# Optimization experiments

Measured on AMD Instinct MI355X. Metric: run time of the kernel, lower is better.

## Reference

```python
import jax, jax.numpy as jnp
import numpy as np

B, T, H, W, D, NH = 8, 16, 14, 14, 768, 12
HID = int(D * 4.0)
HEAD_DIM = D // NH
EPS = 1e-5


def _ln(x, w, b):
    m = x.mean(-1, keepdims=True)
    v = ((x - m) ** 2).mean(-1, keepdims=True)
    return (x - m) * jax.lax.rsqrt(v + EPS) * w + b


def _attn(x, qkv_w, proj_w, proj_b):
    # x: [Bn, S, D]; qkv_w: [D, 3D] (no bias); proj: [D, D] + bias
    Bn, S, _ = x.shape
    qkv = (x @ qkv_w).reshape(Bn, S, 3, NH, HEAD_DIM).transpose(2, 0, 3, 1, 4)
    q, k, v = qkv[0], qkv[1], qkv[2]
    a = jnp.einsum('bhqd,bhkd->bhqk', q, k) * (HEAD_DIM ** -0.5)
    a = jax.nn.softmax(a, axis=-1)
    o = jnp.einsum('bhqk,bhkd->bhqd', a, v).transpose(0, 2, 1, 3).reshape(Bn, S, D)
    return o @ proj_w + proj_b


def setup_inputs() -> dict:
    key = jax.random.key(0)
    ks = jax.random.split(key, 20)
    N = H * W * T
    s = 0.02
    f32 = jnp.float32
    return {
        'x': jax.random.normal(ks[0], (B, 1 + N, D), f32),
        'tn1_w': jnp.ones((D,), f32), 'tn1_b': jnp.zeros((D,), f32),
        't_qkv_w': jax.random.normal(ks[1], (D, 3 * D), f32) * s,
        't_proj_w': jax.random.normal(ks[2], (D, D), f32) * s,
        't_proj_b': jnp.zeros((D,), f32),
        'tfc_w': jax.random.normal(ks[3], (D, D), f32) * s,
        'tfc_b': jnp.zeros((D,), f32),
        'n1_w': jnp.ones((D,), f32), 'n1_b': jnp.zeros((D,), f32),
        's_qkv_w': jax.random.normal(ks[4], (D, 3 * D), f32) * s,
        's_proj_w': jax.random.normal(ks[5], (D, D), f32) * s,
        's_proj_b': jnp.zeros((D,), f32),
        'n2_w': jnp.ones((D,), f32), 'n2_b': jnp.zeros((D,), f32),
        'fc1_w': jax.random.normal(ks[6], (D, HID), f32) * s,
        'fc1_b': jnp.zeros((HID,), f32),
        'fc2_w': jax.random.normal(ks[7], (HID, D), f32) * s,
        'fc2_b': jnp.zeros((D,), f32),
        'pt_mask': jnp.ones((B, 1 + N), dtype=bool),
        't_frames': T, 'height': H, 'width': W,
    }


def reference(x, tn1_w, tn1_b, t_qkv_w, t_proj_w, t_proj_b, tfc_w, tfc_b,
              n1_w, n1_b, s_qkv_w, s_proj_w, s_proj_b, n2_w, n2_b,
              fc1_w, fc1_b, fc2_w, fc2_b, pt_mask, t_frames, height, width):
    # divided space-time attention; USE_CLS_TOKEN=True, use_pt_visibility=False
    b = x.shape[0]
    t, h, w = t_frames, height, width
    n = h * w * t
    # --- temporal attention over t per (b, h, w) ---
    xt = x[:, 1:, :].reshape(b * h * w, t, D)  # 'b (h w t) m -> (b h w) t m'
    rt = _attn(_ln(xt, tn1_w, tn1_b), t_qkv_w, t_proj_w, t_proj_b)
    rt = rt.reshape(b, n, D) @ tfc_w + tfc_b  # temporal_fc
    xt2 = x[:, 1:, :] + rt
    init_cls = x[:, 0:1, :]  # [b, 1, D]
    # --- spatial attention over (1 + h*w) per (b, t) ---
    cls_tok = jnp.broadcast_to(init_cls, (b, t, D)).reshape(b * t, 1, D)
    xs = xt2.reshape(b, h * w, t, D).transpose(0, 2, 1, 3).reshape(b * t, h * w, D)
    xs = jnp.concatenate([cls_tok, xs], axis=1)  # [(b t), 1+hw, D]
    rs = _attn(_ln(xs, n1_w, n1_b), s_qkv_w, s_proj_w, s_proj_b)
    cls_out = rs[:, 0, :].reshape(b, t, D).mean(axis=1, keepdims=True)
    rs = rs[:, 1:, :].reshape(b, t, h * w, D).transpose(0, 2, 1, 3).reshape(b, n, D)
    x_new = jnp.concatenate([init_cls, xt2], axis=1) + jnp.concatenate([cls_out, rs], axis=1)
    # --- MLP block ---
    y = _ln(x_new, n2_w, n2_b)
    y = jax.nn.gelu(y @ fc1_w + fc1_b, approximate=False) @ fc2_w + fc2_b
    return x_new + y
```

## Files before the change

### kernel.cpp

```cpp
#include <hip/hip_runtime.h>
#include <cstdint>

using u16 = unsigned short;
using u32 = unsigned int;

typedef __bf16 bf16x8 __attribute__((ext_vector_type(8)));
typedef float  floatx4 __attribute__((ext_vector_type(4)));

#define DEV static __device__ __forceinline__

DEV u16 f2bf(float f) {
    u32 u = __float_as_uint(f);
    u += 0x7FFFu + ((u >> 16) & 1u);
    return (u16)(u >> 16);
}
DEV float bf2f(u16 v) { return __uint_as_float(((u32)v) << 16); }

DEV floatx4 mfma32(bf16x8 a, bf16x8 b, floatx4 c) {
    return __builtin_amdgcn_mfma_f32_16x16x32_bf16(a, b, c, 0, 0, 0);
}

DEV floatx4 fzero() { floatx4 z; z[0]=0.f; z[1]=0.f; z[2]=0.f; z[3]=0.f; return z; }

typedef __attribute__((address_space(3))) u32 as3_u32;
typedef __attribute__((address_space(1))) u32 as1_u32;

DEV void async_ld16(const u16* g, u16* l) {
    __builtin_amdgcn_global_load_lds(
        (const as1_u32*)g, (as3_u32*)l, 16, 0, 0);
}

__global__ __launch_bounds__(256) void transpose_w(
    const float* __restrict__ W, u16* __restrict__ Wt, int K, int N)
{
    __shared__ float t[32][33];
    const int tx = threadIdx.x, ty = threadIdx.y;
    const int gx = blockIdx.x * 32;
    const int gy = blockIdx.y * 32;
    #pragma unroll
    for (int i = 0; i < 4; ++i)
        t[ty + i*8][tx] = W[(size_t)(gy + ty + i*8) * N + gx + tx];
    __syncthreads();
    #pragma unroll
    for (int i = 0; i < 4; ++i)
        Wt[(size_t)(gx + ty + i*8) * K + gy + tx] = f2bf(t[tx][ty + i*8]);
}

template<int MODE>
__global__ __launch_bounds__(256) void ln_kernel(
    const float* __restrict__ xp, const u16* __restrict__ xt2,
    const float* __restrict__ w, const float* __restrict__ b,
    u16* __restrict__ out, int nrows)
{
    const int row = blockIdx.x * 4 + (threadIdx.x >> 6);
    if (row >= nrows) return;
    const int lane = threadIdx.x & 63;
    float vals[12];
    if constexpr (MODE == 0) {
        const float* src = xp + (size_t)(row + row/3136 + 1) * 768;
        #pragma unroll
        for (int j = 0; j < 3; ++j) {
            float4 v = reinterpret_cast<const float4*>(src)[j*64 + lane];
            vals[j*4+0]=v.x; vals[j*4+1]=v.y; vals[j*4+2]=v.z; vals[j*4+3]=v.w;
        }
    } else {
        const int bt = row / 197;
        const int p  = row - bt * 197;
        const int b0 = bt >> 4, tt = bt & 15;
        if (p == 0) {
            const float* src = xp + (size_t)b0 * 3137 * 768;
            #pragma unroll
            for (int j = 0; j < 3; ++j) {
                float4 v = reinterpret_cast<const float4*>(src)[j*64 + lane];
                vals[j*4+0]=v.x; vals[j*4+1]=v.y; vals[j*4+2]=v.z; vals[j*4+3]=v.w;
            }
        } else {
            const u16* src = xt2 + (size_t)(b0*3136 + (p-1)*16 + tt) * 768;
            #pragma unroll
            for (int j = 0; j < 3; ++j) {
                uint2 q = reinterpret_cast<const uint2*>(src)[j*64 + lane];
                vals[j*4+0] = bf2f((u16)(q.x & 0xFFFF));
                vals[j*4+1] = bf2f((u16)(q.x >> 16));
                vals[j*4+2] = bf2f((u16)(q.y & 0xFFFF));
                vals[j*4+3] = bf2f((u16)(q.y >> 16));
            }
        }
    }
    float s = 0.f, ss = 0.f;
    #pragma unroll
    for (int e = 0; e < 12; ++e) { s += vals[e]; ss += vals[e]*vals[e]; }
    #pragma unroll
    for (int o = 32; o > 0; o >>= 1) { s += __shfl_xor(s, o); ss += __shfl_xor(ss, o); }
    const float mean = s * (1.f/768.f);
    const float var  = ss * (1.f/768.f) - mean*mean;
    const float rstd = rsqrtf(var + 1e-5f);
    #pragma unroll
    for (int j = 0; j < 3; ++j) {
        const int c4 = (j*64 + lane) * 4;
        union { u16 u[4]; uint2 q; } o;
        #pragma unroll
        for (int e = 0; e < 4; ++e)
            o.u[e] = f2bf((vals[j*4+e] - mean)*rstd*w[c4+e] + b[c4+e]);
        *reinterpret_cast<uint2*>(&out[(size_t)row*768 + c4]) = o.q;
    }
}

__global__ __launch_bounds__(256) void combine_ln2(
    const float* __restrict__ xp, const u16* __restrict__ xt2,
    const u16* __restrict__ rsb, const float* __restrict__ w, const float* __restrict__ b,
    float* __restrict__ xnew, u16* __restrict__ ln2, int nrows)
{
    const int row = blockIdx.x * 4 + (threadIdx.x >> 6);
    if (row >= nrows) return;
    const int lane = threadIdx.x & 63;
    const int b0 = row / 3137;
    const int j  = row - b0 * 3137;
    float vals[12];
    if (j == 0) {
        #pragma unroll
        for (int e = 0; e < 12; ++e) {
            const int c = e*64 + lane;
            float acc = 0.f;
            for (int t = 0; t < 16; ++t)
                acc += bf2f(rsb[(size_t)(b0*16 + t) * 197 * 768 + c]);
            vals[e] = xp[(size_t)row*768 + c] + acc * (1.f/16.f);
        }
    } else {
        const int n_idx = j - 1;
        const int hw = n_idx >> 4, tt = n_idx & 15;
        const u16* a  = xt2 + (size_t)(b0*3136 + n_idx) * 768;
        const u16* r2 = rsb + (size_t)((b0*16 + tt)*197 + 1 + hw) * 768;
        #pragma unroll
        for (int e = 0; e < 12; ++e) {
            const int c = e*64 + lane;
            vals[e] = bf2f(a[c]) + bf2f(r2[c]);
        }
    }
    float s = 0.f, ss = 0.f;
    #pragma unroll
    for (int e = 0; e < 12; ++e) { s += vals[e]; ss += vals[e]*vals[e]; }
    #pragma unroll
    for (int o = 32; o > 0; o >>= 1) { s += __shfl_xor(s, o); ss += __shfl_xor(ss, o); }
    const float mean = s * (1.f/768.f);
    const float var  = ss * (1.f/768.f) - mean*mean;
    const float rstd = rsqrtf(var + 1e-5f);
    #pragma unroll
    for (int e = 0; e < 12; ++e) {
        const int c = e*64 + lane;
        xnew[(size_t)row*768 + c] = vals[e];
        ln2[(size_t)row*768 + c]  = f2bf((vals[e] - mean)*rstd*w[c] + b[c]);
    }
}

template<int RESID, bool BIAS, bool GELU_ACT, bool OUTF, bool OUTB, bool MASKM>
__global__ __launch_bounds__(256) void gemm_bt(
    const u16* __restrict__ A, const u16* __restrict__ Bt,
    const float* __restrict__ bias, const float* __restrict__ resid,
    float* __restrict__ Cf, u16* __restrict__ Cb,
    int N, int K, int lda, int ldb, int Mvalid)
{
    __shared__ __attribute__((aligned(16))) u16 smem[2*128*32];
    u16* As = smem;
    u16* Bs = smem + 128*32;
    const int tid  = threadIdx.x;
    const int wave = tid >> 6;
    const int lane = tid & 63;
    const int m15  = lane & 15;
    const int quad = lane >> 4;
    const int wm = wave >> 1, wn = wave & 1;
    const long m0 = (long)blockIdx.y * 128;
    const long n0 = (long)blockIdx.x * 128;

    const int s0 = wave*128 + lane;
    const int s1 = s0 + 64;
    const int kc0 = (s0 & 3) ^ ((s0 >> 3) & 3);
    const int kc1 = (s1 & 3) ^ ((s1 >> 3) & 3);
    const u16* Ag0 = A  + (size_t)(m0 + (s0 >> 2)) * lda + kc0 * 8;
    const u16* Ag1 = A  + (size_t)(m0 + (s1 >> 2)) * lda + kc1 * 8;
    const u16* Bg0 = Bt + (size_t)(n0 + (s0 >> 2)) * ldb + kc0 * 8;
    const u16* Bg1 = Bt + (size_t)(n0 + (s1 >> 2)) * ldb + kc1 * 8;
    u16* Al0 = &As[(wave*2 + 0) * 512];
    u16* Al1 = &As[(wave*2 + 1) * 512];
    u16* Bl0 = &Bs[(wave*2 + 0) * 512];
    u16* Bl1 = &Bs[(wave*2 + 1) * 512];

    const int swz = (quad ^ ((m15 >> 1) & 3)) * 8;

    floatx4 acc[4][4];
    #pragma unroll
    for (int i = 0; i < 4; ++i)
        #pragma unroll
        for (int j = 0; j < 4; ++j) acc[i][j] = fzero();

    for (int k0 = 0; k0 < K; k0 += 32) {
        __syncthreads();
        async_ld16(Ag0 + k0, Al0);
        async_ld16(Ag1 + k0, Al1);
        async_ld16(Bg0 + k0, Bl0);
        async_ld16(Bg1 + k0, Bl1);
        __syncthreads();
        bf16x8 af[4], bf[4];
        #pragma unroll
        for (int i = 0; i < 4; ++i)
            af[i] = *reinterpret_cast<const bf16x8*>(&As[(wm*64 + i*16 + m15)*32 + swz]);
        #pragma unroll
        for (int j = 0; j < 4; ++j)
            bf[j] = *reinterpret_cast<const bf16x8*>(&Bs[(wn*64 + j*16 + m15)*32 + swz]);
        #pragma unroll
        for (int i = 0; i < 4; ++i)
            #pragma unroll
            for (int j = 0; j < 4; ++j)
                acc[i][j] = mfma32(af[i], bf[j], acc[i][j]);
    }

    float bv[4];
    #pragma unroll
    for (int j = 0; j < 4; ++j)
        bv[j] = BIAS ? bias[n0 + wn*64 + j*16 + m15] : 0.f;

    if constexpr (OUTB) {
        u16* cbuf = smem + wave * 2048;
        #pragma unroll
        for (int p = 0; p < 2; ++p) {
            __syncthreads();
            #pragma unroll
            for (int ii = 0; ii < 2; ++ii) {
                const int i = p*2 + ii;
                #pragma unroll
                for (int j = 0; j < 4; ++j) {
                    #pragma unroll
                    for (int r = 0; r < 4; ++r) {
                        const long row = m0 + wm*64 + i*16 + quad*4 + r;
                        float v = acc[i][j][r] + bv[j];
                        if constexpr (RESID == 1)
                            v += resid[(size_t)row * N + (n0 + wn*64 + j*16 + m15)];
                        if constexpr (RESID == 2)
                            v += resid[(size_t)(row + row/3136 + 1) * 768 + (n0 + wn*64 + j*16 + m15)];
                        if constexpr (GELU_ACT)
                            v = 0.5f * v * (1.f + erff(v * 0.70710678118f));
                        cbuf[(ii*16 + quad*4 + r)*64 + j*16 + m15] = f2bf(v);
                    }
                }
            }
            __syncthreads();
            #pragma unroll
            for (int it = 0; it < 4; ++it) {
                const int lr = (lane >> 3) + it*8;
                const int cc = lane & 7;
                const uint4 val = *reinterpret_cast<const uint4*>(&cbuf[lr*64 + cc*8]);
                const long grow = m0 + wm*64 + p*32 + lr;
                *reinterpret_cast<uint4*>(&Cb[(size_t)grow * N + n0 + wn*64 + cc*8]) = val;
            }
        }
    } else {
        #pragma unroll
        for (int j = 0; j < 4; ++j) {
            const long col = n0 + wn*64 + j*16 + m15;
            #pragma unroll
            for (int i = 0; i < 4; ++i) {
                const long rowb = m0 + wm*64 + i*16 + quad*4;
                #pragma unroll
                for (int r = 0; r < 4; ++r) {
                    const long row = rowb + r;
                    if constexpr (MASKM) { if (row >= Mvalid) continue; }
                    float v = acc[i][j][r] + bv[j];
                    if constexpr (RESID == 1) v += resid[(size_t)row * N + col];
                    if constexpr (RESID == 2) v += resid[(size_t)(row + row/3136 + 1) * 768 + col];
                    if constexpr (GELU_ACT)   v = 0.5f * v * (1.f + erff(v * 0.70710678118f));
                    if constexpr (OUTF) Cf[(size_t)row * N + col] = v;
                }
            }
        }
    }
}

template<int S, int NQ, int NIT>
__global__ __launch_bounds__(256) void attn_kernel(
    const u16* __restrict__ qkv, u16* __restrict__ out, int ntask)
{
    __shared__ __attribute__((aligned(16))) u16 P_lds[4][16*32];
    const int wave = threadIdx.x >> 6;
    const int lane = threadIdx.x & 63;
    const int task = blockIdx.x * 4 + wave;
    if (task >= ntask) return;
    const int seq  = task / (12 * NQ);
    const int rem  = task - seq * (12 * NQ);
    const int head = rem / NQ;
    const int qt   = rem - head * NQ;
    const int m15  = lane & 15;
    const int quad = lane >> 4;
    const size_t base = (size_t)seq * S;

    const u16* qp = qkv + (base + qt*16 + m15) * 2304 + head*64 + quad*8;
    const bf16x8 Qf0 = *reinterpret_cast<const bf16x8*>(qp);
    const bf16x8 Qf1 = *reinterpret_cast<const bf16x8*>(qp + 32);

    floatx4 Oacc[4];
    #pragma unroll
    for (int c = 0; c < 4; ++c) Oacc[c] = fzero();
    float mrun = -__builtin_inff();
    float lrun = 0.f;
    u16* P = &P_lds[wave][0];

    for (int it = 0; it < NIT; ++it) {
        const int j0 = it * 32;
        floatx4 st[2];
        #pragma unroll
        for (int h2 = 0; h2 < 2; ++h2) {
            const u16* kp = qkv + (base + j0 + h2*16 + m15) * 2304 + 768 + head*64 + quad*8;
            const bf16x8 K0 = *reinterpret_cast<const bf16x8*>(kp);
            const bf16x8 K1 = *reinterpret_cast<const bf16x8*>(kp + 32);
            floatx4 z = fzero();
            z = mfma32(K0, Qf0, z);
            st[h2] = mfma32(K1, Qf1, z);
        }
        float sc[8];
        #pragma unroll
        for (int h2 = 0; h2 < 2; ++h2)
            #pragma unroll
            for (int r = 0; r < 4; ++r) {
                const int jj = j0 + h2*16 + quad*4 + r;
                sc[h2*4+r] = (jj < S) ? st[h2][r] * 0.125f : -__builtin_inff();
            }
        float tmax = sc[0];
        #pragma unroll
        for (int k = 1; k < 8; ++k) tmax = fmaxf(tmax, sc[k]);
        tmax = fmaxf(tmax, __shfl_xor(tmax, 16));
        tmax = fmaxf(tmax, __shfl_xor(tmax, 32));
        const float mnew = fmaxf(mrun, tmax);
        float p[8], tsum = 0.f;
        #pragma unroll
        for (int k = 0; k < 8; ++k) { p[k] = __expf(sc[k] - mnew); tsum += p[k]; }
        tsum += __shfl_xor(tsum, 16);
        tsum += __shfl_xor(tsum, 32);
        const float alpha = __expf(mrun - mnew);
        lrun = lrun * alpha + tsum;
        mrun = mnew;
        #pragma unroll
        for (int r = 0; r < 4; ++r) {
            const float ar = __shfl(alpha, quad*4 + r);
            #pragma unroll
            for (int c = 0; c < 4; ++c) Oacc[c][r] *= ar;
        }
        #pragma unroll
        for (int h2 = 0; h2 < 2; ++h2)
            #pragma unroll
            for (int r = 0; r < 4; ++r)
                P[m15*32 + h2*16 + quad*4 + r] = f2bf(p[h2*4+r]);
        const bf16x8 Pf = *reinterpret_cast<const bf16x8*>(&P[m15*32 + quad*8]);
        #pragma unroll
        for (int c = 0; c < 4; ++c) {
            union { u16 u[8]; bf16x8 v; } vf;
            #pragma unroll
            for (int jj2 = 0; jj2 < 8; ++jj2)
                vf.u[jj2] = qkv[(base + j0 + quad*8 + jj2) * 2304 + 1536 + head*64 + c*16 + m15];
            Oacc[c] = mfma32(Pf, vf.v, Oacc[c]);
        }
    }
    const float linv_self = 1.f / lrun;
    #pragma unroll
    for (int r = 0; r < 4; ++r) {
        const int prow = qt*16 + quad*4 + r;
        const float linv = __shfl(linv_self, quad*4 + r);
        if (prow < S) {
            u16* op = out + (base + prow) * 768 + head*64 + m15;
            #pragma unroll
            for (int c = 0; c < 4; ++c) op[c*16] = f2bf(Oacc[c][r] * linv);
        }
    }
}

extern "C" void kernel_launch(void* const* d_in, const int* in_sizes, int n_in,
                              void* d_out, int out_size, void* d_ws, size_t ws_size,
                              hipStream_t stream)
{
    (void)in_sizes; (void)n_in; (void)out_size; (void)ws_size;
    const float* x        = (const float*)d_in[0];
    const float* tn1_w    = (const float*)d_in[1];
    const float* tn1_b    = (const float*)d_in[2];
    const float* t_qkv_w  = (const float*)d_in[3];
    const float* t_proj_w = (const float*)d_in[4];
    const float* t_proj_b = (const float*)d_in[5];
    const float* tfc_w    = (const float*)d_in[6];
    const float* tfc_b    = (const float*)d_in[7];
    const float* n1_w     = (const float*)d_in[8];
    const float* n1_b     = (const float*)d_in[9];
    const float* s_qkv_w  = (const float*)d_in[10];
    const float* s_proj_w = (const float*)d_in[11];
    const float* s_proj_b = (const float*)d_in[12];
    const float* n2_w     = (const float*)d_in[13];
    const float* n2_b     = (const float*)d_in[14];
    const float* fc1_w    = (const float*)d_in[15];
    const float* fc1_b    = (const float*)d_in[16];
    const float* fc2_w    = (const float*)d_in[17];
    const float* fc2_b    = (const float*)d_in[18];
    float* out = (float*)d_out;

    char* ws = (char*)d_ws;
    size_t off = 0;
    auto alloc = [&](size_t bytes) -> void* {
        void* p = ws + off;
        off += (bytes + 255) & ~(size_t)255;
        return p;
    };
    u16* wt_tqkv  = (u16*)alloc((size_t)768*2304*2);
    u16* wt_tproj = (u16*)alloc((size_t)768*768*2);
    u16* wt_tfc   = (u16*)alloc((size_t)768*768*2);
    u16* wt_sqkv  = (u16*)alloc((size_t)768*2304*2);
    u16* wt_sproj = (u16*)alloc((size_t)768*768*2);
    u16* wt_fc1   = (u16*)alloc((size_t)768*3072*2);
    u16* wt_fc2   = (u16*)alloc((size_t)3072*768*2);
    u16* slotA = (u16*)alloc((size_t)25280*2304*2);
    u16* slotB = (u16*)alloc((size_t)25216*768*2);
    u16* slotD = (u16*)alloc((size_t)25216*768*2);
    u16* slotE = (u16*)alloc((size_t)25216*768*2);

    dim3 tb(32, 8);
    transpose_w<<<dim3(72, 24), tb, 0, stream>>>(t_qkv_w,  wt_tqkv,  768, 2304);
    transpose_w<<<dim3(24, 24), tb, 0, stream>>>(t_proj_w, wt_tproj, 768, 768);
    transpose_w<<<dim3(24, 24), tb, 0, stream>>>(tfc_w,    wt_tfc,   768, 768);
    transpose_w<<<dim3(72, 24), tb, 0, stream>>>(s_qkv_w,  wt_sqkv,  768, 2304);
    transpose_w<<<dim3(24, 24), tb, 0, stream>>>(s_proj_w, wt_sproj, 768, 768);
    transpose_w<<<dim3(96, 24), tb, 0, stream>>>(fc1_w,    wt_fc1,   768, 3072);
    transpose_w<<<dim3(24, 96), tb, 0, stream>>>(fc2_w,    wt_fc2,   3072, 768);

    u16* lnT  = slotD;
    u16* qkvT = slotA;
    ln_kernel<0><<<25088/4, 256, 0, stream>>>(x, nullptr, tn1_w, tn1_b, lnT, 25088);
    gemm_bt<0,false,false,false,true,false><<<dim3(18,196), 256, 0, stream>>>(
        lnT, wt_tqkv, nullptr, nullptr, nullptr, qkvT, 2304, 768, 768, 768, 0);

    u16* attnT = slotD;
    attn_kernel<16,1,1><<<18816/4, 256, 0, stream>>>(qkvT, attnT, 18816);

    u16* hp = slotE;
    gemm_bt<0,true,false,false,true,false><<<dim3(6,196), 256, 0, stream>>>(
        attnT, wt_tproj, t_proj_b, nullptr, nullptr, hp, 768, 768, 768, 768, 0);

    u16* xt2 = slotB;
    gemm_bt<2,true,false,false,true,false><<<dim3(6,196), 256, 0, stream>>>(
        hp, wt_tfc, tfc_b, x, nullptr, xt2, 768, 768, 768, 768, 0);

    u16* lnS = slotD;
    ln_kernel<1><<<25216/4, 256, 0, stream>>>(x, xt2, n1_w, n1_b, lnS, 25216);

    u16* qkvS = slotA;
    gemm_bt<0,false,false,false,true,false><<<dim3(18,197), 256, 0, stream>>>(
        lnS, wt_sqkv, nullptr, nullptr, nullptr, qkvS, 2304, 768, 768, 768, 0);

    u16* attnS = slotD;
    attn_kernel<197,13,7><<<19968/4, 256, 0, stream>>>(qkvS, attnS, 19968);

    u16* rsb = slotE;
    gemm_bt<0,true,false,false,true,false><<<dim3(6,197), 256, 0, stream>>>(
        attnS, wt_sproj, s_proj_b, nullptr, nullptr, rsb, 768, 768, 768, 768, 0);

    float* xnew = out;
    u16* ln2 = slotD;
    combine_ln2<<<25096/4, 256, 0, stream>>>(x, xt2, rsb, n2_w, n2_b, xnew, ln2, 25096);

    u16* h1 = slotA;
    for (int half = 0; half < 2; ++half) {
        const u16* w1h = wt_fc1 + (size_t)half * 1536 * 768;
        const float* b1h = fc1_b + half * 1536;
        gemm_bt<0,true,true,false,true,false><<<dim3(12,197), 256, 0, stream>>>(
            ln2, w1h, b1h, nullptr, nullptr, h1, 1536, 768, 768, 768, 0);
        const u16* w2h = wt_fc2 + (size_t)half * 1536;
        if (half == 0)
            gemm_bt<1,true,false,true,false,true><<<dim3(6,197), 256, 0, stream>>>(
                h1, w2h, fc2_b, out, out, nullptr, 768, 1536, 1536, 3072, 25096);
        else
            gemm_bt<1,false,false,true,false,true><<<dim3(6,197), 256, 0, stream>>>(
                h1, w2h, nullptr, out, out, nullptr, 768, 1536, 1536, 3072, 25096);
    }
}
```

Baseline: 1.417 ms.

## Replace 128x128 GEMM with 256x256 double-buffered pipelined 8-wave kernel

Replaces the 4-wave 128x128 GEMM, which synchronised around every 32-wide K step, with a 512-thread 256x256 tile kernel. It uses 64-wide K stages double-buffered in 128KB of dynamic LDS, interleaves async global loads with MFMA quarters, and adds explicit waitcnt, sched barriers and setprio. The goal is to hide load latency and raise operand reuse per byte loaded. In exchange it adds M-masking for partial tiles, padding of one slot, and heavy register and LDS pressure that may limit occupancy.

Result: faster. 1.297 ms (-8.4%).

```diff
diff --git a/kernel.cpp b/kernel.cpp
--- a/kernel.cpp
+++ b/kernel.cpp
@@ -152,118 +152,172 @@
     }
 }
 
+
+#define BARX() do { __builtin_amdgcn_sched_barrier(0); asm volatile("" ::: "memory"); \
+    __builtin_amdgcn_s_barrier(); asm volatile("" ::: "memory"); \
+    __builtin_amdgcn_sched_barrier(0); } while(0)
+#define WAITL() do { asm volatile("s_waitcnt lgkmcnt(0)" ::: "memory"); \
+    __builtin_amdgcn_sched_barrier(0); } while(0)
+#define WAITV4() do { asm volatile("s_waitcnt vmcnt(4)" ::: "memory"); \
+    __builtin_amdgcn_sched_barrier(0); } while(0)
+#define WAITV0() do { asm volatile("s_waitcnt vmcnt(0)" ::: "memory"); \
+    __builtin_amdgcn_sched_barrier(0); } while(0)
+
+#define RD_A(d, mh) do { \
+    _Pragma("unroll") for (int ff = 0; ff < 4; ++ff) { \
+      _Pragma("unroll") for (int ks = 0; ks < 2; ++ks) { \
+        const int rr = ((mh)*4 + ff)*16 + m15; \
+        a[ff*2+ks] = *reinterpret_cast<const bf16x8*>( \
+            &sm[(d)*32768 + wm*8192 + rr*64 + ((ks*4 + quad) ^ (m15 & 7))*8]); \
+    } } } while(0)
+
+#define RD_B(d, np) do { \
+    _Pragma("unroll") for (int nn = 0; nn < 2; ++nn) { \
+      _Pragma("unroll") for (int ks = 0; ks < 2; ++ks) { \
+        const int rr = (wn & 1)*64 + ((np)*2 + nn)*16 + m15; \
+        b[((np)*2 + nn)*2 + ks] = *reinterpret_cast<const bf16x8*>( \
+            &sm[(d)*32768 + 16384 + (wn >> 1)*8192 + rr*64 + ((ks*4 + quad) ^ (m15 & 7))*8]); \
+    } } } while(0)
+
+#define MQ(F0, NF0) do { \
+    _Pragma("unroll") for (int ff = 0; ff < 4; ++ff) { \
+      _Pragma("unroll") for (int nn = 0; nn < 2; ++nn) { \
+        floatx4 c_ = acc[(F0)+ff][(NF0)+nn]; \
+        c_ = mfma32(a[ff*2+0], b[((NF0)+nn)*2+0], c_); \
+        c_ = mfma32(a[ff*2+1], b[((NF0)+nn)*2+1], c_); \
+        acc[(F0)+ff][(NF0)+nn] = c_; \
+    } } } while(0)
+
+#define PRIO1() __builtin_amdgcn_s_setprio(1)
+#define PRIO0() __builtin_amdgcn_s_setprio(0)
+
+#define ITER(tt, FULL) do { \
+    const int d_ = (tt) & 1; \
+     RD_A(d_, 0); RD_B(d_, 0); STAGE((tt)+1, 2); \
+    BARX(); WAITL(); PRIO1(); MQ(0,0); PRIO0(); BARX(); \
+     RD_B(d_, 1); STAGE((tt)+1, 3); \
+    BARX(); WAITL(); PRIO1(); MQ(0,2); PRIO0(); BARX(); \
+     RD_A(d_, 1); if (FULL) STAGE((tt)+2, 0); \
+    BARX(); WAITL(); PRIO1(); MQ(4,2); PRIO0(); BARX(); \
+     if (FULL) STAGE((tt)+2, 1); \
+    BARX(); PRIO1(); MQ(4,0); PRIO0(); \
+    if (FULL) WAITV4(); else WAITV0(); \
+    BARX(); \
+     RD_A(d_^1, 0); RD_B(d_^1, 0); if (FULL) STAGE((tt)+2, 2); \
+    BARX(); WAITL(); PRIO1(); MQ(0,0); PRIO0(); BARX(); \
+     RD_B(d_^1, 1); if (FULL) STAGE((tt)+2, 3); \
+    BARX(); WAITL(); PRIO1(); MQ(0,2); PRIO0(); BARX(); \
+     RD_A(d_^1, 1); if (FULL) STAGE((tt)+3, 0); \
+    BARX(); WAITL(); PRIO1(); MQ(4,2); PRIO0(); BARX(); \
+     if (FULL) STAGE((tt)+3, 1); \
+    BARX(); PRIO1(); MQ(4,0); PRIO0(); \
+    if (FULL) WAITV4(); \
+    BARX(); \
+} while(0)
+
 template<int RESID, bool BIAS, bool GELU_ACT, bool OUTF, bool OUTB, bool MASKM>
-__global__ __launch_bounds__(256) void gemm_bt(
+__global__ __launch_bounds__(512, 2) void gemm256(
     const u16* __restrict__ A, const u16* __restrict__ Bt,
     const float* __restrict__ bias, const float* __restrict__ resid,
     float* __restrict__ Cf, u16* __restrict__ Cb,
     int N, int K, int lda, int ldb, int Mvalid)
 {
-    __shared__ __attribute__((aligned(16))) u16 smem[2*128*32];
-    u16* As = smem;
-    u16* Bs = smem + 128*32;
+    extern __shared__ u16 sm[];
     const int tid  = threadIdx.x;
-    const int wave = tid >> 6;
-    const int lane = tid & 63;
-    const int m15  = lane & 15;
-    const int quad = lane >> 4;
-    const int wm = wave >> 1, wn = wave & 1;
-    const long m0 = (long)blockIdx.y * 128;
-    const long n0 = (long)blockIdx.x * 128;
-
-    const int s0 = wave*128 + lane;
-    const int s1 = s0 + 64;
-    const int kc0 = (s0 & 3) ^ ((s0 >> 3) & 3);
-    const int kc1 = (s1 & 3) ^ ((s1 >> 3) & 3);
-    const u16* Ag0 = A  + (size_t)(m0 + (s0 >> 2)) * lda + kc0 * 8;
-    const u16* Ag1 = A  + (size_t)(m0 + (s1 >> 2)) * lda + kc1 * 8;
-    const u16* Bg0 = Bt + (size_t)(n0 + (s0 >> 2)) * ldb + kc0 * 8;
-    const u16* Bg1 = Bt + (size_t)(n0 + (s1 >> 2)) * ldb + kc1 * 8;
-    u16* Al0 = &As[(wave*2 + 0) * 512];
-    u16* Al1 = &As[(wave*2 + 1) * 512];
-    u16* Bl0 = &Bs[(wave*2 + 0) * 512];
-    u16* Bl1 = &Bs[(wave*2 + 1) * 512];
-
-    const int swz = (quad ^ ((m15 >> 1) & 3)) * 8;
-
-    floatx4 acc[4][4];
-    #pragma unroll
-    for (int i = 0; i < 4; ++i)
-        #pragma unroll
-        for (int j = 0; j < 4; ++j) acc[i][j] = fzero();
-
-    for (int k0 = 0; k0 < K; k0 += 32) {
-        __syncthreads();
-        async_ld16(Ag0 + k0, Al0);
-        async_ld16(Ag1 + k0, Al1);
-        async_ld16(Bg0 + k0, Bl0);
-        async_ld16(Bg1 + k0, Bl1);
-        __syncthreads();
-        bf16x8 af[4], bf[4];
-        #pragma unroll
-        for (int i = 0; i < 4; ++i)
-            af[i] = *reinterpret_cast<const bf16x8*>(&As[(wm*64 + i*16 + m15)*32 + swz]);
-        #pragma unroll
-        for (int j = 0; j < 4; ++j)
-            bf[j] = *reinterpret_cast<const bf16x8*>(&Bs[(wn*64 + j*16 + m15)*32 + swz]);
-        #pragma unroll
-        for (int i = 0; i < 4; ++i)
-            #pragma unroll
-            for (int j = 0; j < 4; ++j)
-                acc[i][j] = mfma32(af[i], bf[j], acc[i][j]);
-    }
+    const int w    = tid >> 6;
+    const int l    = tid & 63;
+    const int m15  = l & 15;
+    const int quad = l >> 4;
+    const int wm   = w >> 2;
+    const int wn   = w & 3;
+    const long m0  = (long)blockIdx.y * 256;
+    const long n0  = (long)blockIdx.x * 256;
+
+    const int srow   = w*8 + (l >> 3);
+    const int schunk = ((l & 7) ^ (l >> 3)) * 8;
+    const u16* gA = A  + (size_t)(m0 + srow) * lda + schunk;
+    const u16* gB = Bt + (size_t)(n0 + srow) * ldb + schunk;
+    const int w512 = w * 512;
+
+    auto STAGE = [&](int tt, int h4) {
+        const int dd = tt & 1;
+        const int k0 = tt << 6;
+        const int h  = h4 & 1;
+        if (h4 & 2) {
+            const u16* g = gA + (size_t)(h * 128) * lda + k0;
+            u16* lp = sm + dd*32768 + h*8192 + w512;
+            async_ld16(g, lp);
+            async_ld16(g + (size_t)(64 * lda), lp + 4096);
+        } else {
+            const u16* g = gB + (size_t)(h * 128) * ldb + k0;
+            u16* lp = sm + dd*32768 + 16384 + h*8192 + w512;
+            async_ld16(g, lp);
+            async_ld16(g + (size_t)(64 * ldb), lp + 4096);
+        }
+    };
+
+    bf16x8 a[8], b[8];
+    floatx4 acc[8][4];
+    #pragma unroll
+    for (int f = 0; f < 8; ++f)
+        #pragma unroll
+        for (int nf = 0; nf < 4; ++nf) acc[f][nf] = fzero();
+
+    const int NIT = K >> 7;
+
+    STAGE(0, 0); STAGE(0, 1); STAGE(0, 2); STAGE(0, 3);
+    STAGE(1, 0); STAGE(1, 1);
+    WAITV4(); BARX();
+
+    int t = 0;
+    for (int i = 0; i < NIT - 1; ++i, t += 2) { ITER(t, 1); }
+    ITER(t, 0);
 
     float bv[4];
     #pragma unroll
-    for (int j = 0; j < 4; ++j)
-        bv[j] = BIAS ? bias[n0 + wn*64 + j*16 + m15] : 0.f;
+    for (int nf = 0; nf < 4; ++nf)
+        bv[nf] = BIAS ? bias[n0 + wn*64 + nf*16 + m15] : 0.f;
 
     if constexpr (OUTB) {
-        u16* cbuf = smem + wave * 2048;
-        #pragma unroll
-        for (int p = 0; p < 2; ++p) {
-            __syncthreads();
-            #pragma unroll
-            for (int ii = 0; ii < 2; ++ii) {
-                const int i = p*2 + ii;
+        u16* cst = sm + w * 8192;
+        #pragma unroll
+        for (int f = 0; f < 8; ++f) {
+            #pragma unroll
+            for (int nf = 0; nf < 4; ++nf) {
                 #pragma unroll
-                for (int j = 0; j < 4; ++j) {
-                    #pragma unroll
-                    for (int r = 0; r < 4; ++r) {
-                        const long row = m0 + wm*64 + i*16 + quad*4 + r;
-                        float v = acc[i][j][r] + bv[j];
-                        if constexpr (RESID == 1)
-                            v += resid[(size_t)row * N + (n0 + wn*64 + j*16 + m15)];
-                        if constexpr (RESID == 2)
-                            v += resid[(size_t)(row + row/3136 + 1) * 768 + (n0 + wn*64 + j*16 + m15)];
-                        if constexpr (GELU_ACT)
-                            v = 0.5f * v * (1.f + erff(v * 0.70710678118f));
-                        cbuf[(ii*16 + quad*4 + r)*64 + j*16 + m15] = f2bf(v);
-                    }
+                for (int r = 0; r < 4; ++r) {
+                    const long row = m0 + wm*128 + f*16 + quad*4 + r;
+                    float v = acc[f][nf][r] + bv[nf];
+                    if constexpr (RESID == 1)
+                        v += resid[(size_t)row * N + (n0 + wn*64 + nf*16 + m15)];
+                    if constexpr (RESID == 2)
+                        v += resid[(size_t)(row + row/3136 + 1) * 768 + (n0 + wn*64 + nf*16 + m15)];
+                    if constexpr (GELU_ACT)
+                        v = 0.5f * v * (1.f + erff(v * 0.70710678118f));
+                    cst[(f*16 + quad*4 + r)*64 + nf*16 + m15] = f2bf(v);
                 }
             }
-            __syncthreads();
-            #pragma unroll
-            for (int it = 0; it < 4; ++it) {
-                const int lr = (lane >> 3) + it*8;
-                const int cc = lane & 7;
-                const uint4 val = *reinterpret_cast<const uint4*>(&cbuf[lr*64 + cc*8]);
-                const long grow = m0 + wm*64 + p*32 + lr;
-                *reinterpret_cast<uint4*>(&Cb[(size_t)grow * N + n0 + wn*64 + cc*8]) = val;
-            }
+        }
+        #pragma unroll
+        for (int it = 0; it < 16; ++it) {
+            const int lr = it*8 + (l >> 3);
+            const long grow = m0 + wm*128 + lr;
+            if constexpr (MASKM) { if (grow >= Mvalid) continue; }
+            const int cc = (l & 7) * 8;
+            *reinterpret_cast<uint4*>(&Cb[(size_t)grow * N + n0 + wn*64 + cc]) =
+                *reinterpret_cast<const uint4*>(&cst[lr*64 + cc]);
         }
     } else {
         #pragma unroll
-        for (int j = 0; j < 4; ++j) {
-            const long col = n0 + wn*64 + j*16 + m15;
-            #pragma unroll
-            for (int i = 0; i < 4; ++i) {
-                const long rowb = m0 + wm*64 + i*16 + quad*4;
+        for (int f = 0; f < 8; ++f) {
+            #pragma unroll
+            for (int nf = 0; nf < 4; ++nf) {
+                const long col = n0 + wn*64 + nf*16 + m15;
                 #pragma unroll
                 for (int r = 0; r < 4; ++r) {
-                    const long row = rowb + r;
+                    const long row = m0 + wm*128 + f*16 + quad*4 + r;
                     if constexpr (MASKM) { if (row >= Mvalid) continue; }
-                    float v = acc[i][j][r] + bv[j];
+                    float v = acc[f][nf][r] + bv[nf];
                     if constexpr (RESID == 1) v += resid[(size_t)row * N + col];
                     if constexpr (RESID == 2) v += resid[(size_t)(row + row/3136 + 1) * 768 + col];
                     if constexpr (GELU_ACT)   v = 0.5f * v * (1.f + erff(v * 0.70710678118f));
@@ -412,7 +466,7 @@
     u16* wt_fc2   = (u16*)alloc((size_t)3072*768*2);
     u16* slotA = (u16*)alloc((size_t)25280*2304*2);
     u16* slotB = (u16*)alloc((size_t)25216*768*2);
-    u16* slotD = (u16*)alloc((size_t)25216*768*2);
+    u16* slotD = (u16*)alloc((size_t)25344*768*2);
     u16* slotE = (u16*)alloc((size_t)25216*768*2);
 
     dim3 tb(32, 8);
@@ -424,36 +478,38 @@
     transpose_w<<<dim3(96, 24), tb, 0, stream>>>(fc1_w,    wt_fc1,   768, 3072);
     transpose_w<<<dim3(24, 96), tb, 0, stream>>>(fc2_w,    wt_fc2,   3072, 768);
 
+    const size_t GLDS = 131072;
+
     u16* lnT  = slotD;
     u16* qkvT = slotA;
     ln_kernel<0><<<25088/4, 256, 0, stream>>>(x, nullptr, tn1_w, tn1_b, lnT, 25088);
-    gemm_bt<0,false,false,false,true,false><<<dim3(18,196), 256, 0, stream>>>(
+    gemm256<0,false,false,false,true,false><<<dim3(9,98), 512, GLDS, stream>>>(
         lnT, wt_tqkv, nullptr, nullptr, nullptr, qkvT, 2304, 768, 768, 768, 0);
 
     u16* attnT = slotD;
     attn_kernel<16,1,1><<<18816/4, 256, 0, stream>>>(qkvT, attnT, 18816);
 
     u16* hp = slotE;
-    gemm_bt<0,true,false,false,true,false><<<dim3(6,196), 256, 0, stream>>>(
+    gemm256<0,true,false,false,true,false><<<dim3(3,98), 512, GLDS, stream>>>(
         attnT, wt_tproj, t_proj_b, nullptr, nullptr, hp, 768, 768, 768, 768, 0);
 
     u16* xt2 = slotB;
-    gemm_bt<2,true,false,false,true,false><<<dim3(6,196), 256, 0, stream>>>(
+    gemm256<2,true,false,false,true,false><<<dim3(3,98), 512, GLDS, stream>>>(
         hp, wt_tfc, tfc_b, x, nullptr, xt2, 768, 768, 768, 768, 0);
 
     u16* lnS = slotD;
     ln_kernel<1><<<25216/4, 256, 0, stream>>>(x, xt2, n1_w, n1_b, lnS, 25216);
 
     u16* qkvS = slotA;
-    gemm_bt<0,false,false,false,true,false><<<dim3(18,197), 256, 0, stream>>>(
-        lnS, wt_sqkv, nullptr, nullptr, nullptr, qkvS, 2304, 768, 768, 768, 0);
+    gemm256<0,false,false,false,true,true><<<dim3(9,99), 512, GLDS, stream>>>(
+        lnS, wt_sqkv, nullptr, nullptr, nullptr, qkvS, 2304, 768, 768, 768, 25216);
 
     u16* attnS = slotD;
     attn_kernel<197,13,7><<<19968/4, 256, 0, stream>>>(qkvS, attnS, 19968);
 
     u16* rsb = slotE;
-    gemm_bt<0,true,false,false,true,false><<<dim3(6,197), 256, 0, stream>>>(
-        attnS, wt_sproj, s_proj_b, nullptr, nullptr, rsb, 768, 768, 768, 768, 0);
+    gemm256<0,true,false,false,true,true><<<dim3(3,99), 512, GLDS, stream>>>(
+        attnS, wt_sproj, s_proj_b, nullptr, nullptr, rsb, 768, 768, 768, 768, 25216);
 
     float* xnew = out;
     u16* ln2 = slotD;
@@ -463,14 +519,14 @@
     for (int half = 0; half < 2; ++half) {
         const u16* w1h = wt_fc1 + (size_t)half * 1536 * 768;
         const float* b1h = fc1_b + half * 1536;
-        gemm_bt<0,true,true,false,true,false><<<dim3(12,197), 256, 0, stream>>>(
-            ln2, w1h, b1h, nullptr, nullptr, h1, 1536, 768, 768, 768, 0);
+        gemm256<0,true,true,false,true,true><<<dim3(6,99), 512, GLDS, stream>>>(
+            ln2, w1h, b1h, nullptr, nullptr, h1, 1536, 768, 768, 768, 25096);
         const u16* w2h = wt_fc2 + (size_t)half * 1536;
         if (half == 0)
-            gemm_bt<1,true,false,true,false,true><<<dim3(6,197), 256, 0, stream>>>(
+            gemm256<1,true,false,true,false,true><<<dim3(3,99), 512, GLDS, stream>>>(
                 h1, w2h, fc2_b, out, out, nullptr, 768, 1536, 1536, 3072, 25096);
         else
-            gemm_bt<1,false,false,true,false,true><<<dim3(6,197), 256, 0, stream>>>(
+            gemm256<1,false,false,true,false,true><<<dim3(3,99), 512, GLDS, stream>>>(
                 h1, w2h, nullptr, out, out, nullptr, 768, 1536, 1536, 3072, 25096);
     }
 }
```
